# Performance work log

Hardware: AMD Instinct MI355X
Metric: run time of the kernel (lower is better)

## Reference

```python
import jax, jax.numpy as jnp
import numpy as np

B, N, D = 16, 4096, 256
EPS = 1e-6


def setup_inputs() -> dict:
    key = jax.random.key(0)
    kq, kk, kv, kwq, kwk, kbq, kbk = jax.random.split(key, 7)
    s = 1.0 / np.sqrt(D)
    return {
        "Q": jax.random.normal(kq, (B, N, D), dtype=jnp.float32),
        "K": jax.random.normal(kk, (B, N, D), dtype=jnp.float32),
        "V": jax.random.normal(kv, (B, N, D), dtype=jnp.float32),
        "Wq": jax.random.normal(kwq, (D, D), dtype=jnp.float32) * s,
        "bq": jax.random.normal(kbq, (D,), dtype=jnp.float32) * 0.01,
        "Wk": jax.random.normal(kwk, (D, D), dtype=jnp.float32) * s,
        "bk": jax.random.normal(kbk, (D,), dtype=jnp.float32) * 0.01,
    }


def reference(Q, K, V, Wq, bq, Wk, bk):
    # phi feature maps: sigmoid(Linear(dim, dim)) as in Flow-Attention
    phi_q = jax.nn.sigmoid(jnp.einsum("bnd,de->bne", Q, Wq) + bq)  # [B,N,D]
    phi_k = jax.nn.sigmoid(jnp.einsum("bnd,de->bne", K, Wk) + bk)  # [B,N,D]
    # O: column-normalized phi_k (over sequence); I: row-normalized phi_q (over features)
    O = phi_k / (jnp.sum(phi_k, axis=1, keepdims=True) + EPS)  # [B,N,D]
    I = phi_q / (jnp.sum(phi_q, axis=2, keepdims=True) + EPS)  # [B,N,D]
    # competition over the sequence dim
    V_b = jax.nn.softmax(O * V, axis=1)  # [B,N,D]
    # linear attention: (phi_k^T @ V_b) is the small [B,D,D] state
    KV = jnp.einsum("bnd,bne->bde", phi_k, V_b)  # [B,D,D]
    A = jnp.einsum("bnd,bde->bne", I, KV)  # [B,N,D]
    # sigmoid allocation gate
    R = jax.nn.sigmoid(jnp.sum(phi_q, axis=2, keepdims=True)) * A
    return R
```

## Files before the change

kernel.cpp:

```cpp
#include <hip/hip_runtime.h>
#include <cstddef>

#define EPS_ 1e-6f

typedef unsigned short u16;
typedef __attribute__((ext_vector_type(8))) short short8;
typedef __attribute__((ext_vector_type(8))) unsigned short us8;
typedef __attribute__((ext_vector_type(4))) unsigned short us4;
typedef __attribute__((ext_vector_type(4))) float f32x4;

__device__ __forceinline__ float sigmoidf_(float x){ return 1.0f/(1.0f+__expf(-x)); }
__device__ __forceinline__ u16 f2bf(float x){
  union { float f; unsigned i; } c; c.f = x;
  unsigned r = c.i + 0x7FFFu + ((c.i >> 16) & 1u);
  return (u16)(r >> 16);
}
__device__ __forceinline__ float bf2f(u16 u){
  union { unsigned i; float f; } c; c.i = ((unsigned)u) << 16; return c.f;
}

__global__ __launch_bounds__(256) void prep_w(const float* __restrict__ Wq,
                                              const float* __restrict__ Wk,
                                              u16* __restrict__ WqT,
                                              u16* __restrict__ WkT){
  const int e = blockIdx.x & 255;
  const float* W = (blockIdx.x < 256) ? Wq : Wk;
  u16* WT = (blockIdx.x < 256) ? WqT : WkT;
  const int d = threadIdx.x;
  WT[e*256 + d] = f2bf(W[d*256 + e]);
}

__global__ __launch_bounds__(512, 4) void phi_both(
    const float* __restrict__ Q, const float* __restrict__ K,
    const u16* __restrict__ WqT, const u16* __restrict__ WkT,
    const float* __restrict__ bq, const float* __restrict__ bk,
    u16* __restrict__ phi_q, u16* __restrict__ phi_kT,
    float* __restrict__ rowsum, float* __restrict__ colsum)
{
  __shared__ union {
    u16 A[128][264];
    u16 S[128][264];
    u16 T[256][136];
  } sh;

  const int t = threadIdx.x;
  const int l = t & 63;
  const int w = t >> 6;
  const int wm = w & 1;
  const int wf = w >> 1;
  const int i16 = l & 15, q = l >> 4;
  const int row0 = blockIdx.x * 128;
  const bool trans = (blockIdx.z != 0);

  const float* X    = trans ? K   : Q;
  const u16*  WT    = trans ? WkT : WqT;
  const float* bias = trans ? bk  : bq;

  {
    const int r0 = t >> 4;
    const int c0 = t & 15;
    #pragma unroll
    for (int p2 = 0; p2 < 4; p2++) {
      #pragma unroll
      for (int p1 = 0; p1 < 4; p1++) {
        const int row = r0 + 32*p2;
        const int k4  = c0 + 16*p1;
        float4 v = *(const float4*)&X[(size_t)(row0 + row)*256 + k4*4];
        us4 h; h[0]=f2bf(v.x); h[1]=f2bf(v.y); h[2]=f2bf(v.z); h[3]=f2bf(v.w);
        *(us4*)&sh.A[row][k4*4] = h;
      }
    }
  }
  __syncthreads();

  f32x4 acc[4][4];
  #pragma unroll
  for (int i=0;i<4;i++)
    #pragma unroll
    for (int j=0;j<4;j++) acc[i][j] = (f32x4){0.f,0.f,0.f,0.f};

  const u16* wb = WT + (size_t)(wf*64 + i16)*256 + q*8;
  short8 Bfr[2][4];
  #pragma unroll
  for (int fi=0;fi<4;fi++) Bfr[0][fi] = *(const short8*)&wb[fi*4096];

  #pragma unroll
  for (int it = 0; it < 8; it++) {
    if (it < 7) {
      #pragma unroll
      for (int fi=0;fi<4;fi++)
        Bfr[(it+1)&1][fi] = *(const short8*)&wb[fi*4096 + (it+1)*32];
    }
    short8 af[4];
    #pragma unroll
    for (int mi=0;mi<4;mi++)
      af[mi] = *(const short8*)&sh.A[wm*64 + mi*16 + i16][it*32 + q*8];
    #pragma unroll
    for (int mi=0;mi<4;mi++)
      #pragma unroll
      for (int fi=0;fi<4;fi++)
        acc[mi][fi] = __builtin_amdgcn_mfma_f32_16x16x32_bf16(af[mi], Bfr[it&1][fi], acc[mi][fi], 0,0,0);
  }

  float bv[4];
  #pragma unroll
  for (int fi=0;fi<4;fi++) bv[fi] = bias[wf*64 + fi*16 + i16];

  __syncthreads();

  if (!trans) {
    #pragma unroll
    for (int mi=0;mi<4;mi++) {
      float rs[4] = {0.f,0.f,0.f,0.f};
      #pragma unroll
      for (int fi=0;fi<4;fi++) {
        #pragma unroll
        for (int r=0;r<4;r++) {
          float ph = sigmoidf_(acc[mi][fi][r] + bv[fi]);
          rs[r] += ph;
          sh.S[wm*64 + mi*16 + q*4 + r][wf*64 + fi*16 + i16] = f2bf(ph);
        }
      }
      #pragma unroll
      for (int r=0;r<4;r++) {
        float s = rs[r];
        s += __shfl_xor(s,1); s += __shfl_xor(s,2); s += __shfl_xor(s,4); s += __shfl_xor(s,8);
        if (i16 == 0) atomicAdd(&rowsum[row0 + wm*64 + mi*16 + q*4 + r], s);
      }
    }
    __syncthreads();
    const int row = t >> 2;
    #pragma unroll
    for (int p=0;p<8;p++) {
      const int off = (t&3)*8 + p*32;
      *(us8*)&phi_q[(size_t)(row0 + row)*256 + off] = *(const us8*)&sh.S[row][off];
    }
  } else {
    const int b  = row0 >> 12;
    const int nb = row0 & 4095;
    #pragma unroll
    for (int fi=0;fi<4;fi++) {
      float cp = 0.f;
      #pragma unroll
      for (int mi=0;mi<4;mi++) {
        #pragma unroll
        for (int r=0;r<4;r++) {
          float ph = sigmoidf_(acc[mi][fi][r] + bv[fi]);
          cp += ph;
          sh.T[wf*64 + fi*16 + i16][wm*64 + mi*16 + q*4 + r] = f2bf(ph);
        }
      }
      cp += __shfl_xor(cp,16); cp += __shfl_xor(cp,32);
      if (l < 16) atomicAdd(&colsum[b*256 + wf*64 + fi*16 + i16], cp);
    }
    __syncthreads();
    #pragma unroll
    for (int p2=0;p2<2;p2++) {
      const int f = (t >> 2) + 128*p2;
      #pragma unroll
      for (int p=0;p<4;p++) {
        const int off = (t&3)*8 + p*32;
        *(us8*)&phi_kT[(size_t)(b*256 + f)*4096 + nb + off] = *(const us8*)&sh.T[f][off];
      }
    }
  }
}

__global__ __launch_bounds__(256) void kv_kernel(const u16* __restrict__ phi_kT,
    const float* __restrict__ V, const float* __restrict__ colsum,
    u16* __restrict__ parts, float* __restrict__ denom)
{
  __shared__ u16 phiT_lds[256][72];
  __shared__ u16 E_lds[64][72];

  const int t = threadIdx.x;
  const int l = t & 63;
  const int w = t >> 6;
  const int e0 = blockIdx.x * 64;
  const int nc = blockIdx.y;
  const int b  = blockIdx.z;
  const int nbase = nc * 256;
  const int i16 = l & 15, q = l >> 4;

  const int sd = t >> 3;
  const int sn = (t & 7) * 8;

  us8  rA[8];
  float rV[16];
  #pragma unroll
  for (int p=0;p<8;p++)
    rA[p] = *(const us8*)&phi_kT[(size_t)(b*256 + sd + 32*p)*4096 + nbase + sn];
  #pragma unroll
  for (int j=0;j<16;j++)
    rV[j] = V[(size_t)(b*4096 + nbase + w*16 + j)*256 + e0 + l];

  const float inv_cs = 1.0f / (colsum[b*256 + e0 + l] + EPS_);
  float dsum = 0.f;

  f32x4 acc[4][4];
  #pragma unroll
  for (int i=0;i<4;i++)
    #pragma unroll
    for (int j=0;j<4;j++) acc[i][j] = (f32x4){0.f,0.f,0.f,0.f};

  for (int c = 0; c < 4; c++) {
    #pragma unroll
    for (int p=0;p<8;p++) *(us8*)&phiT_lds[sd + 32*p][sn] = rA[p];
    __syncthreads();
    const int n0n = nbase + (c+1)*64;
    if (c < 3) {
      #pragma unroll
      for (int p=0;p<8;p++)
        rA[p] = *(const us8*)&phi_kT[(size_t)(b*256 + sd + 32*p)*4096 + n0n + sn];
    }
    us8 pv0 = *(const us8*)&phiT_lds[e0 + l][w*16];
    us8 pv1 = *(const us8*)&phiT_lds[e0 + l][w*16 + 8];
    us8 ev0, ev1;
    #pragma unroll
    for (int j=0;j<8;j++) {
      float ef = __expf(bf2f(pv0[j]) * inv_cs * rV[j]);
      dsum += ef; ev0[j] = f2bf(ef);
    }
    #pragma unroll
    for (int j=0;j<8;j++) {
      float ef = __expf(bf2f(pv1[j]) * inv_cs * rV[8+j]);
      dsum += ef; ev1[j] = f2bf(ef);
    }
    *(us8*)&E_lds[l][w*16]     = ev0;
    *(us8*)&E_lds[l][w*16 + 8] = ev1;
    if (c < 3) {
      #pragma unroll
      for (int j=0;j<16;j++)
        rV[j] = V[(size_t)(b*4096 + n0n + w*16 + j)*256 + e0 + l];
    }
    __syncthreads();
    #pragma unroll
    for (int kk=0;kk<2;kk++){
      const int ko = kk*32 + q*8;
      short8 af[4], bfr[4];
      #pragma unroll
      for (int mi=0;mi<4;mi++) af[mi]  = *(const short8*)&phiT_lds[w*64 + mi*16 + i16][ko];
      #pragma unroll
      for (int ei=0;ei<4;ei++) bfr[ei] = *(const short8*)&E_lds[ei*16 + i16][ko];
      #pragma unroll
      for (int mi=0;mi<4;mi++)
        #pragma unroll
        for (int ei=0;ei<4;ei++)
          acc[mi][ei] = __builtin_amdgcn_mfma_f32_16x16x32_bf16(af[mi], bfr[ei], acc[mi][ei],0,0,0);
    }
    __syncthreads();
  }

  atomicAdd(&denom[b*256 + e0 + l], dsum);

  u16* slice = parts + ((size_t)(nc*16 + b)) * 65536;
  #pragma unroll
  for (int mi=0;mi<4;mi++)
    #pragma unroll
    for (int ei=0;ei<4;ei++)
      #pragma unroll
      for (int r=0;r<4;r++)
        slice[(size_t)(w*64 + mi*16 + q*4 + r)*256 + e0 + ei*16 + i16] = f2bf(acc[mi][ei][r]);
}

__global__ __launch_bounds__(256) void kv_norm(const u16* __restrict__ parts,
    const float* __restrict__ denom, u16* __restrict__ KV_nT)
{
  __shared__ float tile[64][65];
  const int t = threadIdx.x;
  const int d0 = blockIdx.x*64, e0 = blockIdx.y*64, b = blockIdx.z;
  const int i = t >> 4, jq = t & 15;
  #pragma unroll
  for (int p=0;p<4;p++){
    int dl = p*16 + i;
    float s0=0.f,s1=0.f,s2=0.f,s3=0.f;
    for (int nc=0;nc<16;nc++){
      us4 v = *(const us4*)&parts[(((size_t)(nc*16 + b))*256 + d0 + dl)*256 + e0 + jq*4];
      s0+=bf2f(v[0]); s1+=bf2f(v[1]); s2+=bf2f(v[2]); s3+=bf2f(v[3]);
    }
    tile[dl][jq*4+0]=s0; tile[dl][jq*4+1]=s1; tile[dl][jq*4+2]=s2; tile[dl][jq*4+3]=s3;
  }
  __syncthreads();
  const int el = t >> 4, dq = t & 15;
  #pragma unroll
  for (int p=0;p<4;p++){
    int e = p*16 + el;
    float dn = denom[b*256 + e0 + e];
    us4 o;
    #pragma unroll
    for (int r=0;r<4;r++) o[r] = f2bf(tile[dq*4+r][e] / dn);
    *(us4*)&KV_nT[((size_t)(b*256 + e0 + e))*256 + d0 + dq*4] = o;
  }
}

__global__ __launch_bounds__(512, 4) void out_gemm(const u16* __restrict__ phi_q,
    const u16* __restrict__ KV_nT, const float* __restrict__ rowsum,
    float* __restrict__ outp)
{
  __shared__ u16 A_lds[128][264];
  __shared__ float rs_lds[128];

  const int t = threadIdx.x;
  const int l = t & 63;
  const int w = t >> 6;
  const int wm = w & 1, we = w >> 1;
  const int i16 = l & 15, q = l >> 4;
  const int n0 = blockIdx.x * 128;
  const int b  = blockIdx.y;

  if (t < 128) rs_lds[t] = rowsum[b*4096 + n0 + t];

  {
    const int row = t >> 2;
    #pragma unroll
    for (int p=0;p<8;p++) {
      const int off = (t&3)*8 + p*32;
      *(us8*)&A_lds[row][off] = *(const us8*)&phi_q[(size_t)(b*4096 + n0 + row)*256 + off];
    }
  }
  __syncthreads();

  f32x4 acc[4][4];
  #pragma unroll
  for (int i=0;i<4;i++)
    #pragma unroll
    for (int j=0;j<4;j++) acc[i][j] = (f32x4){0.f,0.f,0.f,0.f};

  const u16* kb = KV_nT + (size_t)(b*256 + we*64 + i16)*256 + q*8;
  short8 Bfr[2][4];
  #pragma unroll
  for (int ei=0;ei<4;ei++) Bfr[0][ei] = *(const short8*)&kb[ei*4096];

  #pragma unroll
  for (int it=0; it<8; it++){
    if (it < 7) {
      #pragma unroll
      for (int ei=0;ei<4;ei++)
        Bfr[(it+1)&1][ei] = *(const short8*)&kb[ei*4096 + (it+1)*32];
    }
    short8 af[4];
    #pragma unroll
    for (int mi=0;mi<4;mi++)
      af[mi] = *(const short8*)&A_lds[wm*64 + mi*16 + i16][it*32 + q*8];
    #pragma unroll
    for (int mi=0;mi<4;mi++)
      #pragma unroll
      for (int ei=0;ei<4;ei++)
        acc[mi][ei] = __builtin_amdgcn_mfma_f32_16x16x32_bf16(af[mi], Bfr[it&1][ei], acc[mi][ei],0,0,0);
  }

  #pragma unroll
  for (int mi=0;mi<4;mi++){
    #pragma unroll
    for (int r=0;r<4;r++){
      const int nl = wm*64 + mi*16 + q*4 + r;
      float rs = rs_lds[nl];
      float gate = sigmoidf_(rs) / (rs + EPS_);
      #pragma unroll
      for (int ei=0;ei<4;ei++)
        outp[((size_t)(b*4096 + n0 + nl))*256 + we*64 + ei*16 + i16] = gate*acc[mi][ei][r];
    }
  }
}

extern "C" void kernel_launch(void* const* d_in, const int* in_sizes, int n_in,
                              void* d_out, int out_size, void* d_ws, size_t ws_size,
                              hipStream_t stream) {
  const float* Q  = (const float*)d_in[0];
  const float* K  = (const float*)d_in[1];
  const float* V  = (const float*)d_in[2];
  const float* Wq = (const float*)d_in[3];
  const float* bq = (const float*)d_in[4];
  const float* Wk = (const float*)d_in[5];
  const float* bk = (const float*)d_in[6];
  float* out = (float*)d_out;

  u16* phi_q  = (u16*)d_ws;
  u16* phi_kT = phi_q + 16777216;
  u16* WqT    = phi_kT + 16777216;
  u16* WkT    = WqT + 65536;
  float* colsum = (float*)(WkT + 65536);
  float* denom  = colsum + 4096;
  float* rowsum = denom + 4096;
  u16* parts  = (u16*)(rowsum + 65536);
  u16* KV_nT  = parts + 16777216;

  hipMemsetAsync(colsum, 0, (4096 + 4096 + 65536) * sizeof(float), stream);

  prep_w<<<dim3(512), 256, 0, stream>>>(Wq, Wk, WqT, WkT);
  phi_both<<<dim3(512, 1, 2), 512, 0, stream>>>(Q, K, WqT, WkT, bq, bk,
                                                phi_q, phi_kT, rowsum, colsum);
  kv_kernel<<<dim3(4, 16, 16), 256, 0, stream>>>(phi_kT, V, colsum, parts, denom);
  kv_norm<<<dim3(4, 4, 16), 256, 0, stream>>>(parts, denom, KV_nT);
  out_gemm<<<dim3(32, 16), 512, 0, stream>>>(phi_q, KV_nT, rowsum, out);
}
```

Before: 319.1 us.

## Use chunked phi_kT layout, transposed partials, smaller GEMM tiles, native bf16 convert

```diff
diff --git a/kernel.cpp b/kernel.cpp
--- a/kernel.cpp
+++ b/kernel.cpp
@@ -11,12 +11,13 @@
 
 __device__ __forceinline__ float sigmoidf_(float x){ return 1.0f/(1.0f+__expf(-x)); }
 __device__ __forceinline__ u16 f2bf(float x){
-  union { float f; unsigned i; } c; c.f = x;
-  unsigned r = c.i + 0x7FFFu + ((c.i >> 16) & 1u);
-  return (u16)(r >> 16);
+  union { __bf16 b; u16 u; } c; c.b = (__bf16)x; return c.u;
 }
 __device__ __forceinline__ float bf2f(u16 u){
   union { unsigned i; float f; } c; c.i = ((unsigned)u) << 16; return c.f;
+}
+__device__ __forceinline__ us4 cvt4(float4 v){
+  us4 h; h[0]=f2bf(v.x); h[1]=f2bf(v.y); h[2]=f2bf(v.z); h[3]=f2bf(v.w); return h;
 }
 
 __global__ __launch_bounds__(256) void prep_w(const float* __restrict__ Wq,
@@ -30,7 +31,7 @@
   WT[e*256 + d] = f2bf(W[d*256 + e]);
 }
 
-__global__ __launch_bounds__(512, 4) void phi_both(
+__global__ __launch_bounds__(256, 4) void phi_both(
     const float* __restrict__ Q, const float* __restrict__ K,
     const u16* __restrict__ WqT, const u16* __restrict__ WkT,
     const float* __restrict__ bq, const float* __restrict__ bk,
@@ -38,18 +39,16 @@
     float* __restrict__ rowsum, float* __restrict__ colsum)
 {
   __shared__ union {
-    u16 A[128][264];
-    u16 S[128][264];
-    u16 T[256][136];
+    u16 A[64][264];
+    u16 S[64][264];
+    u16 T2[128][136];
   } sh;
 
   const int t = threadIdx.x;
   const int l = t & 63;
-  const int w = t >> 6;
-  const int wm = w & 1;
-  const int wf = w >> 1;
+  const int wf = t >> 6;
   const int i16 = l & 15, q = l >> 4;
-  const int row0 = blockIdx.x * 128;
+  const int row0 = blockIdx.x * 64;
   const bool trans = (blockIdx.z != 0);
 
   const float* X    = trans ? K   : Q;
@@ -63,11 +62,10 @@
     for (int p2 = 0; p2 < 4; p2++) {
       #pragma unroll
       for (int p1 = 0; p1 < 4; p1++) {
-        const int row = r0 + 32*p2;
+        const int row = r0 + 16*p2;
         const int k4  = c0 + 16*p1;
         float4 v = *(const float4*)&X[(size_t)(row0 + row)*256 + k4*4];
-        us4 h; h[0]=f2bf(v.x); h[1]=f2bf(v.y); h[2]=f2bf(v.z); h[3]=f2bf(v.w);
-        *(us4*)&sh.A[row][k4*4] = h;
+        *(us4*)&sh.A[row][k4*4] = cvt4(v);
       }
     }
   }
@@ -94,7 +92,7 @@
     short8 af[4];
     #pragma unroll
     for (int mi=0;mi<4;mi++)
-      af[mi] = *(const short8*)&sh.A[wm*64 + mi*16 + i16][it*32 + q*8];
+      af[mi] = *(const short8*)&sh.A[mi*16 + i16][it*32 + q*8];
     #pragma unroll
     for (int mi=0;mi<4;mi++)
       #pragma unroll
@@ -111,64 +109,67 @@
   if (!trans) {
     #pragma unroll
     for (int mi=0;mi<4;mi++) {
-      float rs[4] = {0.f,0.f,0.f,0.f};
+      float rsub[4] = {0.f,0.f,0.f,0.f};
       #pragma unroll
       for (int fi=0;fi<4;fi++) {
         #pragma unroll
         for (int r=0;r<4;r++) {
           float ph = sigmoidf_(acc[mi][fi][r] + bv[fi]);
-          rs[r] += ph;
-          sh.S[wm*64 + mi*16 + q*4 + r][wf*64 + fi*16 + i16] = f2bf(ph);
+          rsub[r] += ph;
+          sh.S[mi*16 + q*4 + r][wf*64 + fi*16 + i16] = f2bf(ph);
         }
       }
       #pragma unroll
       for (int r=0;r<4;r++) {
-        float s = rs[r];
+        float s = rsub[r];
         s += __shfl_xor(s,1); s += __shfl_xor(s,2); s += __shfl_xor(s,4); s += __shfl_xor(s,8);
-        if (i16 == 0) atomicAdd(&rowsum[row0 + wm*64 + mi*16 + q*4 + r], s);
+        if (i16 == 0) atomicAdd(&rowsum[row0 + mi*16 + q*4 + r], s);
       }
     }
     __syncthreads();
-    const int row = t >> 2;
-    #pragma unroll
-    for (int p=0;p<8;p++) {
-      const int off = (t&3)*8 + p*32;
-      *(us8*)&phi_q[(size_t)(row0 + row)*256 + off] = *(const us8*)&sh.S[row][off];
+    const size_t gbase = (size_t)row0 * 256;
+    #pragma unroll
+    for (int j=0;j<8;j++) {
+      const int g = (j*256 + t) * 8;
+      *(us8*)&phi_q[gbase + g] = *(const us8*)&sh.S[g >> 8][g & 255];
     }
   } else {
-    const int b  = row0 >> 12;
-    const int nb = row0 & 4095;
-    #pragma unroll
-    for (int fi=0;fi<4;fi++) {
-      float cp = 0.f;
-      #pragma unroll
-      for (int mi=0;mi<4;mi++) {
+    const int b      = row0 >> 12;
+    const int nchunk = (row0 & 4095) >> 6;
+    #pragma unroll
+    for (int h = 0; h < 2; h++) {
+      if ((wf >> 1) == h) {
         #pragma unroll
-        for (int r=0;r<4;r++) {
-          float ph = sigmoidf_(acc[mi][fi][r] + bv[fi]);
-          cp += ph;
-          sh.T[wf*64 + fi*16 + i16][wm*64 + mi*16 + q*4 + r] = f2bf(ph);
+        for (int fi=0;fi<4;fi++) {
+          float cp = 0.f;
+          #pragma unroll
+          for (int mi=0;mi<4;mi++) {
+            #pragma unroll
+            for (int r=0;r<4;r++) {
+              float ph = sigmoidf_(acc[mi][fi][r] + bv[fi]);
+              cp += ph;
+              sh.T2[(wf*64 + fi*16 + i16) & 127][mi*16 + q*4 + r] = f2bf(ph);
+            }
+          }
+          cp += __shfl_xor(cp,16); cp += __shfl_xor(cp,32);
+          if (l < 16) atomicAdd(&colsum[b*256 + wf*64 + fi*16 + l], cp);
         }
       }
-      cp += __shfl_xor(cp,16); cp += __shfl_xor(cp,32);
-      if (l < 16) atomicAdd(&colsum[b*256 + wf*64 + fi*16 + i16], cp);
-    }
-    __syncthreads();
-    #pragma unroll
-    for (int p2=0;p2<2;p2++) {
-      const int f = (t >> 2) + 128*p2;
-      #pragma unroll
-      for (int p=0;p<4;p++) {
-        const int off = (t&3)*8 + p*32;
-        *(us8*)&phi_kT[(size_t)(b*256 + f)*4096 + nb + off] = *(const us8*)&sh.T[f][off];
-      }
+      __syncthreads();
+      const size_t gb = ((size_t)(b*64 + nchunk)*256 + h*128) * 64;
+      #pragma unroll
+      for (int j=0;j<4;j++) {
+        const int g = (j*256 + t) * 8;
+        *(us8*)&phi_kT[gb + g] = *(const us8*)&sh.T2[g >> 6][g & 63];
+      }
+      __syncthreads();
     }
   }
 }
 
 __global__ __launch_bounds__(256) void kv_kernel(const u16* __restrict__ phi_kT,
     const float* __restrict__ V, const float* __restrict__ colsum,
-    u16* __restrict__ parts, float* __restrict__ denom)
+    u16* __restrict__ partsT, float* __restrict__ denom)
 {
   __shared__ u16 phiT_lds[256][72];
   __shared__ u16 E_lds[64][72];
@@ -179,20 +180,21 @@
   const int e0 = blockIdx.x * 64;
   const int nc = blockIdx.y;
   const int b  = blockIdx.z;
-  const int nbase = nc * 256;
   const int i16 = l & 15, q = l >> 4;
 
   const int sd = t >> 3;
   const int sn = (t & 7) * 8;
 
+  const size_t cbase = (size_t)(b*64 + nc*4) * 256 * 64;
+
   us8  rA[8];
   float rV[16];
   #pragma unroll
   for (int p=0;p<8;p++)
-    rA[p] = *(const us8*)&phi_kT[(size_t)(b*256 + sd + 32*p)*4096 + nbase + sn];
+    rA[p] = *(const us8*)&phi_kT[cbase + (size_t)(sd + 32*p)*64 + sn];
   #pragma unroll
   for (int j=0;j<16;j++)
-    rV[j] = V[(size_t)(b*4096 + nbase + w*16 + j)*256 + e0 + l];
+    rV[j] = V[(size_t)(b*4096 + nc*256 + w*16 + j)*256 + e0 + l];
 
   const float inv_cs = 1.0f / (colsum[b*256 + e0 + l] + EPS_);
   float dsum = 0.f;
@@ -207,11 +209,11 @@
     #pragma unroll
     for (int p=0;p<8;p++) *(us8*)&phiT_lds[sd + 32*p][sn] = rA[p];
     __syncthreads();
-    const int n0n = nbase + (c+1)*64;
     if (c < 3) {
+      const size_t nb = cbase + (size_t)(c+1)*16384;
       #pragma unroll
       for (int p=0;p<8;p++)
-        rA[p] = *(const us8*)&phi_kT[(size_t)(b*256 + sd + 32*p)*4096 + n0n + sn];
+        rA[p] = *(const us8*)&phi_kT[nb + (size_t)(sd + 32*p)*64 + sn];
     }
     us8 pv0 = *(const us8*)&phiT_lds[e0 + l][w*16];
     us8 pv1 = *(const us8*)&phiT_lds[e0 + l][w*16 + 8];
@@ -231,7 +233,7 @@
     if (c < 3) {
       #pragma unroll
       for (int j=0;j<16;j++)
-        rV[j] = V[(size_t)(b*4096 + n0n + w*16 + j)*256 + e0 + l];
+        rV[j] = V[(size_t)(b*4096 + nc*256 + (c+1)*64 + w*16 + j)*256 + e0 + l];
     }
     __syncthreads();
     #pragma unroll
@@ -253,69 +255,58 @@
 
   atomicAdd(&denom[b*256 + e0 + l], dsum);
 
-  u16* slice = parts + ((size_t)(nc*16 + b)) * 65536;
+  u16* slice = partsT + (size_t)(nc*16 + b) * 65536;
   #pragma unroll
   for (int mi=0;mi<4;mi++)
     #pragma unroll
-    for (int ei=0;ei<4;ei++)
-      #pragma unroll
-      for (int r=0;r<4;r++)
-        slice[(size_t)(w*64 + mi*16 + q*4 + r)*256 + e0 + ei*16 + i16] = f2bf(acc[mi][ei][r]);
-}
-
-__global__ __launch_bounds__(256) void kv_norm(const u16* __restrict__ parts,
+    for (int ei=0;ei<4;ei++) {
+      us4 o;
+      #pragma unroll
+      for (int r=0;r<4;r++) o[r] = f2bf(acc[mi][ei][r]);
+      *(us4*)&slice[(size_t)(e0 + ei*16 + i16)*256 + w*64 + mi*16 + q*4] = o;
+    }
+}
+
+__global__ __launch_bounds__(256) void kv_norm(const u16* __restrict__ partsT,
     const float* __restrict__ denom, u16* __restrict__ KV_nT)
 {
-  __shared__ float tile[64][65];
   const int t = threadIdx.x;
-  const int d0 = blockIdx.x*64, e0 = blockIdx.y*64, b = blockIdx.z;
-  const int i = t >> 4, jq = t & 15;
-  #pragma unroll
-  for (int p=0;p<4;p++){
-    int dl = p*16 + i;
-    float s0=0.f,s1=0.f,s2=0.f,s3=0.f;
-    for (int nc=0;nc<16;nc++){
-      us4 v = *(const us4*)&parts[(((size_t)(nc*16 + b))*256 + d0 + dl)*256 + e0 + jq*4];
-      s0+=bf2f(v[0]); s1+=bf2f(v[1]); s2+=bf2f(v[2]); s3+=bf2f(v[3]);
-    }
-    tile[dl][jq*4+0]=s0; tile[dl][jq*4+1]=s1; tile[dl][jq*4+2]=s2; tile[dl][jq*4+3]=s3;
-  }
-  __syncthreads();
-  const int el = t >> 4, dq = t & 15;
-  #pragma unroll
-  for (int p=0;p<4;p++){
-    int e = p*16 + el;
-    float dn = denom[b*256 + e0 + e];
-    us4 o;
-    #pragma unroll
-    for (int r=0;r<4;r++) o[r] = f2bf(tile[dq*4+r][e] / dn);
-    *(us4*)&KV_nT[((size_t)(b*256 + e0 + e))*256 + d0 + dq*4] = o;
-  }
-}
-
-__global__ __launch_bounds__(512, 4) void out_gemm(const u16* __restrict__ phi_q,
+  const int b = blockIdx.y;
+  const size_t idx = (size_t)blockIdx.x * 1024 + t*4;
+  const int e = (int)(idx >> 8);
+  const float dn = denom[b*256 + e];
+  float s0=0.f,s1=0.f,s2=0.f,s3=0.f;
+  #pragma unroll 4
+  for (int nc=0;nc<16;nc++){
+    us4 v = *(const us4*)&partsT[(size_t)(nc*16 + b)*65536 + idx];
+    s0+=bf2f(v[0]); s1+=bf2f(v[1]); s2+=bf2f(v[2]); s3+=bf2f(v[3]);
+  }
+  us4 o; o[0]=f2bf(s0/dn); o[1]=f2bf(s1/dn); o[2]=f2bf(s2/dn); o[3]=f2bf(s3/dn);
+  *(us4*)&KV_nT[(size_t)b*65536 + idx] = o;
+}
+
+__global__ __launch_bounds__(256, 4) void out_gemm(const u16* __restrict__ phi_q,
     const u16* __restrict__ KV_nT, const float* __restrict__ rowsum,
     float* __restrict__ outp)
 {
-  __shared__ u16 A_lds[128][264];
-  __shared__ float rs_lds[128];
+  __shared__ u16 A_lds[64][264];
+  __shared__ float rs_lds[64];
 
   const int t = threadIdx.x;
   const int l = t & 63;
-  const int w = t >> 6;
-  const int wm = w & 1, we = w >> 1;
+  const int we = t >> 6;
   const int i16 = l & 15, q = l >> 4;
-  const int n0 = blockIdx.x * 128;
+  const int n0 = blockIdx.x * 64;
   const int b  = blockIdx.y;
 
-  if (t < 128) rs_lds[t] = rowsum[b*4096 + n0 + t];
+  if (t < 64) rs_lds[t] = rowsum[b*4096 + n0 + t];
 
   {
-    const int row = t >> 2;
-    #pragma unroll
-    for (int p=0;p<8;p++) {
-      const int off = (t&3)*8 + p*32;
-      *(us8*)&A_lds[row][off] = *(const us8*)&phi_q[(size_t)(b*4096 + n0 + row)*256 + off];
+    const size_t gbase = (size_t)(b*4096 + n0) * 256;
+    #pragma unroll
+    for (int j=0;j<8;j++) {
+      const int g = (j*256 + t) * 8;
+      *(us8*)&A_lds[g >> 8][g & 255] = *(const us8*)&phi_q[gbase + g];
     }
   }
   __syncthreads();
@@ -341,7 +332,7 @@
     short8 af[4];
     #pragma unroll
     for (int mi=0;mi<4;mi++)
-      af[mi] = *(const short8*)&A_lds[wm*64 + mi*16 + i16][it*32 + q*8];
+      af[mi] = *(const short8*)&A_lds[mi*16 + i16][it*32 + q*8];
     #pragma unroll
     for (int mi=0;mi<4;mi++)
       #pragma unroll
@@ -353,9 +344,9 @@
   for (int mi=0;mi<4;mi++){
     #pragma unroll
     for (int r=0;r<4;r++){
-      const int nl = wm*64 + mi*16 + q*4 + r;
-      float rs = rs_lds[nl];
-      float gate = sigmoidf_(rs) / (rs + EPS_);
+      const int nl = mi*16 + q*4 + r;
+      const float rs = rs_lds[nl];
+      const float gate = sigmoidf_(rs) / (rs + EPS_);
       #pragma unroll
       for (int ei=0;ei<4;ei++)
         outp[((size_t)(b*4096 + n0 + nl))*256 + we*64 + ei*16 + i16] = gate*acc[mi][ei][r];
@@ -382,15 +373,15 @@
   float* colsum = (float*)(WkT + 65536);
   float* denom  = colsum + 4096;
   float* rowsum = denom + 4096;
-  u16* parts  = (u16*)(rowsum + 65536);
-  u16* KV_nT  = parts + 16777216;
+  u16* partsT = (u16*)(rowsum + 65536);
+  u16* KV_nT  = partsT + 16777216;
 
   hipMemsetAsync(colsum, 0, (4096 + 4096 + 65536) * sizeof(float), stream);
 
   prep_w<<<dim3(512), 256, 0, stream>>>(Wq, Wk, WqT, WkT);
-  phi_both<<<dim3(512, 1, 2), 512, 0, stream>>>(Q, K, WqT, WkT, bq, bk,
-                                                phi_q, phi_kT, rowsum, colsum);
-  kv_kernel<<<dim3(4, 16, 16), 256, 0, stream>>>(phi_kT, V, colsum, parts, denom);
-  kv_norm<<<dim3(4, 4, 16), 256, 0, stream>>>(parts, denom, KV_nT);
-  out_gemm<<<dim3(32, 16), 512, 0, stream>>>(phi_q, KV_nT, rowsum, out);
-}
+  phi_both<<<dim3(1024, 1, 2), 256, 0, stream>>>(Q, K, WqT, WkT, bq, bk,
+                                                 phi_q, phi_kT, rowsum, colsum);
+  kv_kernel<<<dim3(4, 16, 16), 256, 0, stream>>>(phi_kT, V, colsum, partsT, denom);
+  kv_norm<<<dim3(64, 16), 256, 0, stream>>>(partsT, denom, KV_nT);
+  out_gemm<<<dim3(64, 16), 256, 0, stream>>>(phi_q, KV_nT, rowsum, out);
+}
```

Result: no change. 313.2 us (-1.9%).
